# Optimization experiments

Measured on AMD Instinct MI355X. Metric: run time of the kernel, lower is better.

Reference implementation:

```python
import jax, jax.numpy as jnp
import numpy as np

SHIFT, REDUCE = 1, 2
B, L, E, H = 128, 64, 512, 512
T = 2 * L - 1  # valid binary-parse transition sequence length


def _make_transitions(rng):
    # Random *valid* shift-reduce sequences: L shifts, L-1 reduces, stack ends at 1.
    trans = np.zeros((B, T), dtype=np.int32)
    for b in range(B):
        stack, buf = 0, L
        for t in range(T):
            ops_left = T - t
            can_shift = buf > 0 and stack < ops_left
            can_reduce = stack >= 2
            if can_shift and can_reduce:
                act = SHIFT if rng.random() < 0.5 else REDUCE
            elif can_shift:
                act = SHIFT
            else:
                act = REDUCE
            if act == SHIFT:
                buf -= 1; stack += 1
            else:
                stack -= 1
            trans[b, t] = act
    return trans


def setup_inputs() -> dict:
    key = jax.random.key(0)
    k1, k2, k3, k4 = jax.random.split(key, 4)
    sentence = jax.random.normal(k1, (B, L, E), dtype=jnp.float32)
    transitions = jnp.asarray(_make_transitions(np.random.default_rng(0)))
    W_word = jax.random.normal(k2, (E, 2 * H), dtype=jnp.float32) / np.sqrt(E).astype(np.float32)
    b_word = jnp.zeros((2 * H,), dtype=jnp.float32)
    W_left = jax.random.normal(k3, (H, 5 * H), dtype=jnp.float32) / np.sqrt(H).astype(np.float32)
    W_right = jax.random.normal(k4, (H, 5 * H), dtype=jnp.float32) / np.sqrt(H).astype(np.float32)
    b_reduce = jnp.zeros((5 * H,), dtype=jnp.float32)
    return {"sentence": sentence, "transitions": transitions, "W_word": W_word,
            "b_word": b_word, "W_left": W_left, "W_right": W_right, "b_reduce": b_reduce}


def reference(sentence, transitions, W_word, b_word, W_left, W_right, b_reduce):
    Bx, Lx, _ = sentence.shape
    Hx = W_left.shape[0]
    Tx = transitions.shape[1]
    # word projection (no_batch_norm=True, dropout=0 in this config)
    out = sentence @ W_word + b_word                      # [B, L, 2H]
    h_buf, c_buf = jnp.split(out, 2, axis=2)              # buffers, popped front-to-back
    rows = jnp.arange(Bx)
    ops_left_seq = jnp.arange(Tx, 0, -1, dtype=jnp.int32)
    init = (jnp.zeros((Bx, Lx, Hx), out.dtype),           # stack h
            jnp.zeros((Bx, Lx, Hx), out.dtype),           # stack c
            jnp.zeros((Bx,), jnp.int32),                  # stack ptr
            jnp.zeros((Bx,), jnp.int32))                  # buffer ptr

    def step(carry, xs):
        sh, sc, sp, bp = carry
        act, ops = xs
        act = jnp.where(sp > ops, REDUCE, act)            # forced reduce (discrete stack)
        is_red = act == REDUCE
        is_shf = act == SHIFT
        r_idx = jnp.clip(sp - 1, 0, Lx - 1)
        l_idx = jnp.clip(sp - 2, 0, Lx - 1)
        hl, cl = sh[rows, l_idx], sc[rows, l_idx]
        hr, cr = sh[rows, r_idx], sc[rows, r_idx]
        # TreeLSTM Reduce cell
        gates = hl @ W_left + hr @ W_right + b_reduce     # [B, 5H]
        g, i, f1, f2, o = jnp.split(gates, 5, axis=1)
        c_red = jnp.tanh(g) * jax.nn.sigmoid(i) + jax.nn.sigmoid(f1) * cl + jax.nn.sigmoid(f2) * cr
        h_red = jax.nn.sigmoid(o) * jnp.tanh(c_red)
        b_idx = jnp.clip(bp, 0, Lx - 1)
        h_shf, c_shf = h_buf[rows, b_idx], c_buf[rows, b_idx]
        w_idx = jnp.where(is_red, l_idx, jnp.clip(sp, 0, Lx - 1))
        h_cur, c_cur = sh[rows, w_idx], sc[rows, w_idx]
        m_red, m_shf = is_red[:, None], is_shf[:, None]
        wh = jnp.where(m_red, h_red, jnp.where(m_shf, h_shf, h_cur))
        wc = jnp.where(m_red, c_red, jnp.where(m_shf, c_shf, c_cur))
        sh = sh.at[rows, w_idx].set(wh)
        sc = sc.at[rows, w_idx].set(wc)
        sp = sp + is_shf.astype(jnp.int32) - is_red.astype(jnp.int32)
        bp = bp + is_shf.astype(jnp.int32)
        return (sh, sc, sp, bp), None

    (sh, sc, sp, bp), _ = jax.lax.scan(step, init, (transitions.T, ops_left_seq))
    return sh[rows, jnp.clip(sp - 1, 0, Lx - 1)]          # [B, H] top of each stack
```

## Files before the change

### kernel.cpp

```cpp
#include <hip/hip_runtime.h>
#include <hip/hip_bf16.h>


#define Bn 128
#define Ln 64
#define En 512
#define Hn 512
#define Tn 127
#define LEAF_ROWS (Bn*Ln)
#define NODE_ROWS (Bn*(Ln-1))
#define TOT_ROWS (LEAF_ROWS+NODE_ROWS)
#define NLVL 64
#define NXCD 8
#define CAPX 512
#define NBLK 512
#define FPAD 16
#define MAXRANK 96
#define SPIN_CAP (1<<22)
#define WLDS_BYTES 65536
#define PART_BYTES (4*2*16*20*4)
#define DYN_BYTES (WLDS_BYTES + PART_BYTES)

#define OFF_CENSUS 0
#define OFF_RANK   (OFF_CENSUS + NXCD*FPAD)
#define OFF_SFLAG  (OFF_RANK + NBLK*FPAD)
#define OFF_SGEN   (OFF_SFLAG + NBLK*FPAD)
#define OFF_FX     (OFF_SGEN + FPAD)
#define OFF_GX     (OFF_FX + NXCD*MAXRANK*FPAD)
#define BAR_INTS   (OFF_GX + NXCD*FPAD)

typedef __attribute__((ext_vector_type(8))) short bf16x8;
typedef __attribute__((ext_vector_type(4))) float f32x4;

static __device__ __forceinline__ float bf2f(unsigned short u){
  unsigned v = ((unsigned)u) << 16;
  float f; __builtin_memcpy(&f, &v, 4); return f;
}
static __device__ __forceinline__ unsigned short f2bf(float f){
  unsigned u; __builtin_memcpy(&u, &f, 4);
  u = u + 0x7FFFu + ((u >> 16) & 1u);
  return (unsigned short)(u >> 16);
}
static __device__ __forceinline__ float sigm(float x){
  return 1.0f / (1.0f + __expf(-x));
}
static __device__ __forceinline__ float tanh_fast(float x){
  x = fminf(fmaxf(x, -15.0f), 15.0f);
  float t = __expf(2.0f * x);
  return (t - 1.0f) / (t + 1.0f);
}
static __device__ __forceinline__ int xcc_id(){
  unsigned v;
  asm volatile("s_getreg_b32 %0, hwreg(HW_REG_XCC_ID)" : "=s"(v));
  return (int)(v & 7);
}

static __device__ __forceinline__ void xcd_barrier(int* bar, int x, int rank, int nx, int epoch){
  __syncthreads();
  int* fx = bar + OFF_FX + x * MAXRANK * FPAD;
  int* gx = bar + OFF_GX + x * FPAD;
  int nxl = min(nx, MAXRANK);
  if (rank == 0){
    for (int i = threadIdx.x + 1; i < nxl; i += 256){
      int c = 0;
      while (__hip_atomic_load(&fx[i * FPAD], __ATOMIC_RELAXED, __HIP_MEMORY_SCOPE_AGENT) < epoch && c < SPIN_CAP){
        __builtin_amdgcn_s_sleep(1); ++c;
      }
    }
    __syncthreads();
    if (threadIdx.x == 0)
      __hip_atomic_store(gx, epoch, __ATOMIC_RELAXED, __HIP_MEMORY_SCOPE_AGENT);
  } else {
    if (threadIdx.x == 0){
      __hip_atomic_store(&fx[rank * FPAD], epoch, __ATOMIC_RELAXED, __HIP_MEMORY_SCOPE_AGENT);
      int c = 0;
      while (__hip_atomic_load(gx, __ATOMIC_RELAXED, __HIP_MEMORY_SCOPE_AGENT) < epoch && c < SPIN_CAP){
        __builtin_amdgcn_s_sleep(2); ++c;
      }
    }
    __syncthreads();
  }
  asm volatile("" ::: "memory");
}


__global__ void cvt_vec4(const float4* __restrict__ x, ushort4* __restrict__ y, int n4){
  int i = blockIdx.x * 256 + threadIdx.x;
  if (i < n4){
    float4 v = x[i];
    ushort4 o;
    o.x = f2bf(v.x); o.y = f2bf(v.y); o.z = f2bf(v.z); o.w = f2bf(v.w);
    y[i] = o;
  }
}

__global__ void transpose_cvt(const float* __restrict__ src, unsigned short* __restrict__ dstT,
                              int CS, int DS, int koff){
  __shared__ float tile[32][33];
  int c0 = blockIdx.x * 32, r0 = blockIdx.y * 32;
  int tx = threadIdx.x, ty = threadIdx.y;
  for (int i = ty; i < 32; i += 8) tile[i][tx] = src[(size_t)(r0 + i) * CS + c0 + tx];
  __syncthreads();
  for (int i = ty; i < 32; i += 8)
    dstT[(size_t)(c0 + i) * DS + koff + r0 + tx] = f2bf(tile[tx][i]);
}

__global__ void precompute_ctrl(const int* __restrict__ trans,
                                int* __restrict__ srcL, int* __restrict__ srcR,
                                int* __restrict__ dstv, int* __restrict__ cnt,
                                int* __restrict__ outsrc, int* __restrict__ bar){
  __shared__ int stk[Bn][Ln + 1];
  __shared__ int scnt[NXCD * NLVL];
  __shared__ int smaxl[NXCD];
  int b = threadIdx.x;
  for (int i = b; i < NXCD * NLVL; i += 128) scnt[i] = 0;
  if (b < NXCD) smaxl[b] = 0;
  for (int i = b; i < BAR_INTS; i += 128) bar[i] = 0;
  __syncthreads();
  int x = b & 7;
  int sp = 0, bp = 0, nodecnt = 0;
  int act_next = trans[b * Tn];
  for (int t = 0; t < Tn; t++){
    int act = act_next;
    if (t + 1 < Tn) act_next = trans[b * Tn + t + 1];
    int ops = Tn - t;
    if (sp > ops) act = 2;
    if (act == 2){
      int R = stk[b][sp - 1], L = stk[b][sp - 2];
      int lvl = max(R >> 20, L >> 20) + 1;
      int slot = atomicAdd(&scnt[x * NLVL + lvl], 1);
      int base = (x * NLVL + lvl) * CAPX + slot;
      srcL[base] = (L & 0xFFFFF) * Hn;
      srcR[base] = (R & 0xFFFFF) * Hn;
      int noderow = LEAF_ROWS + b * (Ln - 1) + nodecnt;
      dstv[base] = noderow * Hn;
      stk[b][sp - 2] = noderow | (lvl << 20);
      sp -= 1; nodecnt++;
    } else {
      stk[b][sp] = b * Ln + min(bp, Ln - 1);
      sp += 1; bp += 1;
    }
  }
  int root = stk[b][max(sp - 1, 0)];
  outsrc[b] = (root & 0xFFFFF) * Hn;
  atomicMax(&smaxl[x], root >> 20);
  __syncthreads();
  for (int i = b; i < NXCD * NLVL; i += 128) cnt[i] = scnt[i];
  if (b < NXCD) cnt[NXCD * NLVL + b] = smaxl[b];
}

__global__ __launch_bounds__(256) void word_gemm(
    const unsigned short* __restrict__ SB, const unsigned short* __restrict__ WwT,
    const float* __restrict__ b_word,
    unsigned short* __restrict__ HB, float* __restrict__ CF){
  int nt = blockIdx.x;
  int mt = blockIdx.y;
  int tid = threadIdx.x, w = tid >> 6, lane = tid & 63;
  int wm = w >> 1, wn = w & 1;
  int rc = lane & 15, lg = lane >> 4;
  const unsigned short* ap0 = SB + (size_t)(mt * 64 + wm * 32 + rc) * En + lg * 8;
  const unsigned short* ap1 = ap0 + (size_t)16 * En;
  const unsigned short* bp0 = WwT + (size_t)(nt * 128 + wn * 64 + rc) * En + lg * 8;
  f32x4 acc[2][4];
  #pragma unroll
  for (int h = 0; h < 2; h++)
    #pragma unroll
    for (int nb = 0; nb < 4; nb++) acc[h][nb] = (f32x4){0.f,0.f,0.f,0.f};
  #pragma unroll 4
  for (int k0 = 0; k0 < En; k0 += 32){
    bf16x8 a0 = *(const bf16x8*)(ap0 + k0);
    bf16x8 a1 = *(const bf16x8*)(ap1 + k0);
    #pragma unroll
    for (int nb = 0; nb < 4; nb++){
      bf16x8 bb = *(const bf16x8*)(bp0 + (size_t)nb * 16 * En + k0);
      acc[0][nb] = __builtin_amdgcn_mfma_f32_16x16x32_bf16(a0, bb, acc[0][nb], 0, 0, 0);
      acc[1][nb] = __builtin_amdgcn_mfma_f32_16x16x32_bf16(a1, bb, acc[1][nb], 0, 0, 0);
    }
  }
  #pragma unroll
  for (int nb = 0; nb < 4; nb++){
    int col = nt * 128 + wn * 64 + nb * 16 + rc;
    float bw = b_word[col];
    #pragma unroll
    for (int h = 0; h < 2; h++){
      #pragma unroll
      for (int q = 0; q < 4; q++){
        int row = mt * 64 + wm * 32 + h * 16 + lg * 4 + q;
        float v = acc[h][nb][q] + bw;
        if (col < Hn) HB[(size_t)row * Hn + col] = f2bf(v);
        else          CF[(size_t)row * Hn + (col - Hn)] = v;
      }
    }
  }
}

template<bool LDSB>
static __device__ __forceinline__ void tile64(
    int u0, int t, int nr, const int* __restrict__ sL, const int* __restrict__ sR,
    const int* __restrict__ dl,
    unsigned short* __restrict__ HB, float* __restrict__ CF,
    const unsigned short* __restrict__ WT, const float* __restrict__ b_red,
    const unsigned short* __restrict__ wlds, int rc, int lg)
{
  int base = t * 64;
  int offL[4], offR[4];
  #pragma unroll
  for (int m = 0; m < 4; m++){
    int i = min(base + m * 16 + rc, nr - 1);
    offL[m] = sL[i]; offR[m] = sR[i];
  }
  f32x4 acc[5][4];
  #pragma unroll
  for (int g = 0; g < 5; g++)
    #pragma unroll
    for (int m = 0; m < 4; m++) acc[g][m] = (f32x4){0.f,0.f,0.f,0.f};

  int bswz = (rc & 7) << 3;
  const unsigned short* gb = WT + (size_t)(u0 + rc) * 1024 + lg * 8;

  bf16x8 a_cur[4], b_cur[3];
  #pragma unroll
  for (int m = 0; m < 4; m++) a_cur[m] = *(const bf16x8*)(HB + offL[m] + lg * 8);
  #pragma unroll
  for (int g = 0; g < 3; g++)
    b_cur[g] = *(const bf16x8*)(gb + (size_t)(g + 2) * (512 * 1024));

  #pragma unroll 4
  for (int j = 0; j < 32; ++j){
    bf16x8 a_nxt[4], b_nxt[3];
    if (j < 31){
      int kn = (j + 1) * 32 + lg * 8;
      #pragma unroll
      for (int m = 0; m < 4; m++){
        const unsigned short* ap = (j + 1 < 16) ? (HB + offL[m] + kn) : (HB + offR[m] + (kn - 512));
        a_nxt[m] = *(const bf16x8*)ap;
      }
      #pragma unroll
      for (int g = 0; g < 3; g++)
        b_nxt[g] = *(const bf16x8*)(gb + (size_t)(g + 2) * (512 * 1024) + (j + 1) * 32);
    }
    int k = j * 32 + lg * 8;
    #pragma unroll
    for (int g = 0; g < 2; g++){
      bf16x8 bb;
      if (LDSB) bb = *(const bf16x8*)&wlds[(size_t)(g * 16 + rc) * 1024 + (k ^ bswz)];
      else      bb = *(const bf16x8*)(gb + (size_t)g * (512 * 1024) + j * 32);
      #pragma unroll
      for (int m = 0; m < 4; m++)
        acc[g][m] = __builtin_amdgcn_mfma_f32_16x16x32_bf16(a_cur[m], bb, acc[g][m], 0, 0, 0);
    }
    #pragma unroll
    for (int g = 0; g < 3; g++){
      #pragma unroll
      for (int m = 0; m < 4; m++)
        acc[g + 2][m] = __builtin_amdgcn_mfma_f32_16x16x32_bf16(a_cur[m], b_cur[g], acc[g + 2][m], 0, 0, 0);
    }
    #pragma unroll
    for (int m = 0; m < 4; m++) a_cur[m] = a_nxt[m];
    #pragma unroll
    for (int g = 0; g < 3; g++) b_cur[g] = b_nxt[g];
  }
  int colu = u0 + rc;
  float bs[5];
  #pragma unroll
  for (int g = 0; g < 5; g++) bs[g] = b_red[g * Hn + colu];
  #pragma unroll
  for (int m = 0; m < 4; m++){
    #pragma unroll
    for (int q = 0; q < 4; q++){
      int i = base + m * 16 + lg * 4 + q;
      if (i < nr){
        int oL = sL[i], oR = sR[i], oD = dl[i];
        float gv = tanh_fast(acc[0][m][q] + bs[0]);
        float iv = sigm(acc[1][m][q] + bs[1]);
        float f1 = sigm(acc[2][m][q] + bs[2]);
        float f2 = sigm(acc[3][m][q] + bs[3]);
        float ov = sigm(acc[4][m][q] + bs[4]);
        float cl = __builtin_nontemporal_load(CF + oL + colu);
        float cr = __builtin_nontemporal_load(CF + oR + colu);
        float cv = gv * iv + f1 * cl + f2 * cr;
        float hv = ov * tanh_fast(cv);
        __builtin_nontemporal_store(cv, CF + oD + colu);
        HB[oD + colu] = f2bf(hv);
      }
    }
  }
}

static __device__ __forceinline__ void tile16(
    int u0, int t, int nr, const int* __restrict__ sL, const int* __restrict__ sR,
    const int* __restrict__ dl,
    unsigned short* __restrict__ HB, float* __restrict__ CF,
    const unsigned short* __restrict__ WT, const float* __restrict__ b_red,
    const unsigned short* __restrict__ wlds, float (*part)[2][16][20],
    int tid, int w, int rc, int lg)
{
  int base = t * 16;
  int i0 = min(base + rc, nr - 1);
  int offA = (w >= 2) ? sR[i0] : sL[i0];
  int k0 = w * 256;
  int abase = (w >= 2) ? (k0 - 512) : k0;
  const unsigned short* ap = HB + offA + abase + lg * 8;
  int bswz = (rc & 7) << 3;
  const unsigned short* gb = WT + (size_t)(u0 + rc) * 1024;

  f32x4 acc[5];
  #pragma unroll
  for (int g = 0; g < 5; g++) acc[g] = (f32x4){0.f,0.f,0.f,0.f};

  bf16x8 a_cur = *(const bf16x8*)ap;
  bf16x8 b_cur[3];
  #pragma unroll
  for (int g = 0; g < 3; g++)
    b_cur[g] = *(const bf16x8*)(gb + (size_t)(g + 2) * (512 * 1024) + k0 + lg * 8);

  #pragma unroll
  for (int j = 0; j < 8; ++j){
    bf16x8 a_nxt, b_nxt[3];
    if (j < 7){
      a_nxt = *(const bf16x8*)(ap + (j + 1) * 32);
      #pragma unroll
      for (int g = 0; g < 3; g++)
        b_nxt[g] = *(const bf16x8*)(gb + (size_t)(g + 2) * (512 * 1024) + k0 + (j + 1) * 32 + lg * 8);
    }
    int k = k0 + j * 32 + lg * 8;
    #pragma unroll
    for (int g = 0; g < 2; g++){
      bf16x8 bb = *(const bf16x8*)&wlds[(size_t)(g * 16 + rc) * 1024 + (k ^ bswz)];
      acc[g] = __builtin_amdgcn_mfma_f32_16x16x32_bf16(a_cur, bb, acc[g], 0, 0, 0);
    }
    #pragma unroll
    for (int g = 0; g < 3; g++)
      acc[g + 2] = __builtin_amdgcn_mfma_f32_16x16x32_bf16(a_cur, b_cur[g], acc[g + 2], 0, 0, 0);
    a_cur = a_nxt;
    #pragma unroll
    for (int g = 0; g < 3; g++) b_cur[g] = b_nxt[g];
  }
  int er = tid >> 4, eu = tid & 15;
  float sg[5];
  #pragma unroll
  for (int r = 0; r < 3; ++r){
    int ng = (r < 2) ? 2 : 1;
    #pragma unroll
    for (int gi = 0; gi < 2; ++gi){
      if (gi < ng){
        int g = r * 2 + gi;
        #pragma unroll
        for (int q = 0; q < 4; q++) part[w][gi][lg * 4 + q][rc] = acc[g][q];
      }
    }
    __syncthreads();
    #pragma unroll
    for (int gi = 0; gi < 2; ++gi){
      if (gi < ng)
        sg[r * 2 + gi] = part[0][gi][er][eu] + part[1][gi][er][eu]
                       + part[2][gi][er][eu] + part[3][gi][er][eu];
    }
    __syncthreads();
  }
  int i = base + er;
  if (i < nr){
    int colu = u0 + eu;
    int oL = sL[i], oR = sR[i], oD = dl[i];
    float gv = tanh_fast(sg[0] + b_red[colu]);
    float iv = sigm(sg[1] + b_red[Hn + colu]);
    float f1 = sigm(sg[2] + b_red[2 * Hn + colu]);
    float f2 = sigm(sg[3] + b_red[3 * Hn + colu]);
    float ov = sigm(sg[4] + b_red[4 * Hn + colu]);
    float cl = __builtin_nontemporal_load(CF + oL + colu);
    float cr = __builtin_nontemporal_load(CF + oR + colu);
    float cv = gv * iv + f1 * cl + f2 * cr;
    float hv = ov * tanh_fast(cv);
    __builtin_nontemporal_store(cv, CF + oD + colu);
    HB[oD + colu] = f2bf(hv);
  }
  __syncthreads();
}

extern __shared__ char dynbuf[];

__global__ __launch_bounds__(256, 2) void tree_kernel(
    unsigned short* __restrict__ HB, float* __restrict__ CF,
    const unsigned short* __restrict__ WT, const float* __restrict__ b_red,
    const int* __restrict__ srcL, const int* __restrict__ srcR,
    const int* __restrict__ dstv, const int* __restrict__ cnt,
    const int* __restrict__ outsrc, float* __restrict__ out, int* bar){
  unsigned short* wlds = (unsigned short*)dynbuf;
  float (*part)[2][16][20] = (float(*)[2][16][20])(dynbuf + WLDS_BYTES);
  int bid = blockIdx.x;
  int tid = threadIdx.x, w = tid >> 6, lane = tid & 63;
  int rc = lane & 15, lg = lane >> 4;

  int x = xcc_id();
  if (tid == 0){
    int r = __hip_atomic_fetch_add(&bar[OFF_CENSUS + x * FPAD], 1,
                                   __ATOMIC_RELAXED, __HIP_MEMORY_SCOPE_AGENT);
    __hip_atomic_store(&bar[OFF_RANK + bid * FPAD], r, __ATOMIC_RELAXED, __HIP_MEMORY_SCOPE_AGENT);
  }
  __syncthreads();
  int rank = min(__hip_atomic_load(&bar[OFF_RANK + bid * FPAD], __ATOMIC_RELAXED, __HIP_MEMORY_SCOPE_AGENT),
                 MAXRANK - 1);
  int ub = rank & 31;
  int u0 = ub * 16;

  for (int gg = tid; gg < 4096; gg += 256){
    int row = gg >> 7;
    int k = (gg & 127) * 8;
    int u = row & 15, g = row >> 4;
    bf16x8 v = *(const bf16x8*)(WT + (size_t)(g * 512 + u0 + u) * 1024 + k);
    int kx = k ^ ((u & 7) << 3);
    *(bf16x8*)&wlds[(size_t)row * 1024 + kx] = v;
  }
  __syncthreads();

  {
    int* sfl  = bar + OFF_SFLAG;
    int* sgen = bar + OFF_SGEN;
    if (bid == 0){
      for (int i = tid; i < NBLK; i += 256){
        if (i){
          int c = 0;
          while (__hip_atomic_load(&sfl[i * FPAD], __ATOMIC_RELAXED, __HIP_MEMORY_SCOPE_AGENT) == 0 && c < SPIN_CAP){
            __builtin_amdgcn_s_sleep(1); ++c;
          }
        }
      }
      __syncthreads();
      if (tid == 0) __hip_atomic_store(sgen, 1, __ATOMIC_RELAXED, __HIP_MEMORY_SCOPE_AGENT);
    } else {
      if (tid == 0){
        __hip_atomic_store(&sfl[bid * FPAD], 1, __ATOMIC_RELAXED, __HIP_MEMORY_SCOPE_AGENT);
        int c = 0;
        while (__hip_atomic_load(sgen, __ATOMIC_RELAXED, __HIP_MEMORY_SCOPE_AGENT) == 0 && c < SPIN_CAP){
          __builtin_amdgcn_s_sleep(2); ++c;
        }
      }
      __syncthreads();
    }
  }
  int nx = max(__hip_atomic_load(&bar[OFF_CENSUS + x * FPAD], __ATOMIC_RELAXED, __HIP_MEMORY_SCOPE_AGENT), 1);

  int maxlvl = cnt[NXCD * NLVL + x];
  int epoch = 1;
  for (int lvl = 1; lvl <= maxlvl; ++lvl, ++epoch){
    int nr = cnt[x * NLVL + lvl];
    const int* sL = srcL + (x * NLVL + lvl) * CAPX;
    const int* sR = srcR + (x * NLVL + lvl) * CAPX;
    const int* dl = dstv + (x * NLVL + lvl) * CAPX;
    if (nr > 0){
      if (nx >= 32){
        int nstr = (nx - 1 - ub) / 32 + 1;
        int stripe = rank >> 5;
        if (nr >= 128){
          int ntl = (nr + 63) >> 6;
          for (int t = stripe * 4 + w; t < ntl; t += nstr * 4)
            tile64<true>(u0, t, nr, sL, sR, dl, HB, CF, WT, b_red, wlds, rc, lg);
        } else {
          int ntl16 = (nr + 15) >> 4;
          for (int t = stripe; t < ntl16; t += nstr)
            tile16(u0, t, nr, sL, sR, dl, HB, CF, WT, b_red, wlds, part, tid, w, rc, lg);
        }
      } else {
        int ntl = (nr + 63) >> 6;
        int nwv = nx * 4, wid = rank * 4 + w;
        int ntask = ntl * 32;
        for (int task = wid; task < ntask; task += nwv)
          tile64<false>((task / ntl) * 16, task % ntl, nr, sL, sR, dl, HB, CF, WT, b_red, wlds, rc, lg);
      }
    }
    xcd_barrier(bar, x, rank, nx, epoch);
  }

  for (int j = rank; j < 16; j += min(nx, MAXRANK)){
    int b = x + 8 * j;
    int src = outsrc[b];
    out[b * Hn + tid]       = bf2f(HB[src + tid]);
    out[b * Hn + tid + 256] = bf2f(HB[src + tid + 256]);
  }
}

extern "C" void kernel_launch(void* const* d_in, const int* in_sizes, int n_in,
                              void* d_out, int out_size, void* d_ws, size_t ws_size,
                              hipStream_t stream){
  (void)in_sizes; (void)n_in; (void)out_size; (void)ws_size;
  const float* sentence = (const float*)d_in[0];
  const int*   trans    = (const int*)d_in[1];
  const float* W_word   = (const float*)d_in[2];
  const float* b_word   = (const float*)d_in[3];
  const float* W_left   = (const float*)d_in[4];
  const float* W_right  = (const float*)d_in[5];
  const float* b_red    = (const float*)d_in[6];

  char* ws = (char*)d_ws;
  size_t off = 0;
  auto alloc = [&](size_t bytes) -> void* {
    void* p = ws + off;
    off += (bytes + 255) & ~((size_t)255);
    return p;
  };
  unsigned short* HB  = (unsigned short*)alloc((size_t)TOT_ROWS * Hn * 2);
  float*          CF  = (float*)alloc((size_t)TOT_ROWS * Hn * 4);
  unsigned short* WT  = (unsigned short*)alloc((size_t)2560 * 1024 * 2);
  unsigned short* SB  = (unsigned short*)alloc((size_t)LEAF_ROWS * En * 2);
  unsigned short* WwT = (unsigned short*)alloc((size_t)1024 * En * 2);
  int* srcL   = (int*)alloc((size_t)NXCD * NLVL * CAPX * 4);
  int* srcR   = (int*)alloc((size_t)NXCD * NLVL * CAPX * 4);
  int* dstv   = (int*)alloc((size_t)NXCD * NLVL * CAPX * 4);
  int* cnt    = (int*)alloc((size_t)(NXCD * NLVL + NXCD) * 4);
  int* outsrc = (int*)alloc((size_t)Bn * 4);
  int* bar    = (int*)alloc((size_t)BAR_INTS * 4);
  float* outp = (float*)d_out;

  hipFuncSetAttribute(reinterpret_cast<const void*>(tree_kernel),
                      hipFuncAttributeMaxDynamicSharedMemorySize, DYN_BYTES);

  cvt_vec4<<<(LEAF_ROWS * En / 4) / 256, 256, 0, stream>>>((const float4*)sentence, (ushort4*)SB, LEAF_ROWS * En / 4);
  transpose_cvt<<<dim3(1024 / 32, En / 32), dim3(32, 8), 0, stream>>>(W_word, WwT, 1024, En, 0);
  transpose_cvt<<<dim3(2560 / 32, Hn / 32), dim3(32, 8), 0, stream>>>(W_left, WT, 2560, 1024, 0);
  transpose_cvt<<<dim3(2560 / 32, Hn / 32), dim3(32, 8), 0, stream>>>(W_right, WT, 2560, 1024, 512);
  precompute_ctrl<<<1, 128, 0, stream>>>(trans, srcL, srcR, dstv, cnt, outsrc, bar);
  word_gemm<<<dim3(8, LEAF_ROWS / 64), 256, 0, stream>>>(SB, WwT, b_word, HB, CF);
  tree_kernel<<<NBLK, 256, DYN_BYTES, stream>>>(HB, CF, WT, b_red, srcL, srcR, dstv, cnt, outsrc, outp, bar);
}
```

Baseline: 598.3 us.

## Deepen load pipelines, prefetch next-level indices, hoist cell-state loads, tighten barrier spin

The word GEMM and the tile16 inner loop now use a three-stage register ring that prefetches two k-steps ahead instead of one. Both tree tiles load the child cell states (cl/cr) before the MFMA loop, so that latency overlaps compute. tile16 also cuts its LDS reduction from three sync rounds to two by enlarging the partial buffer. Before each XCD barrier, the next level's index gathers for tile16 are issued early. The barrier spin drops or shortens its sleeps to cut wake-up latency, which adds register pressure and memory polling traffic.

Result: slower. 776.4 us (+29.8%).

```diff
diff --git a/kernel.cpp b/kernel.cpp
--- a/kernel.cpp
+++ b/kernel.cpp
@@ -17,8 +17,9 @@
 #define FPAD 16
 #define MAXRANK 96
 #define SPIN_CAP (1<<22)
+#define GATE_STRIDE (512*1024)
 #define WLDS_BYTES 65536
-#define PART_BYTES (4*2*16*20*4)
+#define PART_BYTES (4*3*16*20*4)
 #define DYN_BYTES (WLDS_BYTES + PART_BYTES)
 
 #define OFF_CENSUS 0
@@ -64,7 +65,7 @@
     for (int i = threadIdx.x + 1; i < nxl; i += 256){
       int c = 0;
       while (__hip_atomic_load(&fx[i * FPAD], __ATOMIC_RELAXED, __HIP_MEMORY_SCOPE_AGENT) < epoch && c < SPIN_CAP){
-        __builtin_amdgcn_s_sleep(1); ++c;
+        ++c;
       }
     }
     __syncthreads();
@@ -75,7 +76,7 @@
       __hip_atomic_store(&fx[rank * FPAD], epoch, __ATOMIC_RELAXED, __HIP_MEMORY_SCOPE_AGENT);
       int c = 0;
       while (__hip_atomic_load(gx, __ATOMIC_RELAXED, __HIP_MEMORY_SCOPE_AGENT) < epoch && c < SPIN_CAP){
-        __builtin_amdgcn_s_sleep(2); ++c;
+        __builtin_amdgcn_s_sleep(1); ++c;
       }
     }
     __syncthreads();
@@ -166,15 +167,31 @@
   for (int h = 0; h < 2; h++)
     #pragma unroll
     for (int nb = 0; nb < 4; nb++) acc[h][nb] = (f32x4){0.f,0.f,0.f,0.f};
-  #pragma unroll 4
-  for (int k0 = 0; k0 < En; k0 += 32){
-    bf16x8 a0 = *(const bf16x8*)(ap0 + k0);
-    bf16x8 a1 = *(const bf16x8*)(ap1 + k0);
+
+  bf16x8 aS0[3], aS1[3], bS[4][3];
+  #pragma unroll
+  for (int s = 0; s < 2; s++){
+    aS0[s] = *(const bf16x8*)(ap0 + s * 32);
+    aS1[s] = *(const bf16x8*)(ap1 + s * 32);
+    #pragma unroll
+    for (int nb = 0; nb < 4; nb++)
+      bS[nb][s] = *(const bf16x8*)(bp0 + (size_t)nb * 16 * En + s * 32);
+  }
+  #pragma unroll
+  for (int j = 0; j < 16; ++j){
+    const int cur = j % 3, n2 = (j + 2) % 3;
+    if (j < 14){
+      int kn = (j + 2) * 32;
+      aS0[n2] = *(const bf16x8*)(ap0 + kn);
+      aS1[n2] = *(const bf16x8*)(ap1 + kn);
+      #pragma unroll
+      for (int nb = 0; nb < 4; nb++)
+        bS[nb][n2] = *(const bf16x8*)(bp0 + (size_t)nb * 16 * En + kn);
+    }
     #pragma unroll
     for (int nb = 0; nb < 4; nb++){
-      bf16x8 bb = *(const bf16x8*)(bp0 + (size_t)nb * 16 * En + k0);
-      acc[0][nb] = __builtin_amdgcn_mfma_f32_16x16x32_bf16(a0, bb, acc[0][nb], 0, 0, 0);
-      acc[1][nb] = __builtin_amdgcn_mfma_f32_16x16x32_bf16(a1, bb, acc[1][nb], 0, 0, 0);
+      acc[0][nb] = __builtin_amdgcn_mfma_f32_16x16x32_bf16(aS0[cur], bS[nb][cur], acc[0][nb], 0, 0, 0);
+      acc[1][nb] = __builtin_amdgcn_mfma_f32_16x16x32_bf16(aS1[cur], bS[nb][cur], acc[1][nb], 0, 0, 0);
     }
   }
   #pragma unroll
@@ -209,6 +226,17 @@
     int i = min(base + m * 16 + rc, nr - 1);
     offL[m] = sL[i]; offR[m] = sR[i];
   }
+  int colu = u0 + rc;
+  float clv[4][4], crv[4][4];
+  #pragma unroll
+  for (int m = 0; m < 4; m++){
+    #pragma unroll
+    for (int q = 0; q < 4; q++){
+      int ic = min(base + m * 16 + lg * 4 + q, nr - 1);
+      clv[m][q] = __builtin_nontemporal_load(CF + sL[ic] + colu);
+      crv[m][q] = __builtin_nontemporal_load(CF + sR[ic] + colu);
+    }
+  }
   f32x4 acc[5][4];
   #pragma unroll
   for (int g = 0; g < 5; g++)
@@ -223,7 +251,7 @@
   for (int m = 0; m < 4; m++) a_cur[m] = *(const bf16x8*)(HB + offL[m] + lg * 8);
   #pragma unroll
   for (int g = 0; g < 3; g++)
-    b_cur[g] = *(const bf16x8*)(gb + (size_t)(g + 2) * (512 * 1024));
+    b_cur[g] = *(const bf16x8*)(gb + (size_t)(g + 2) * GATE_STRIDE);
 
   #pragma unroll 4
   for (int j = 0; j < 32; ++j){
@@ -237,14 +265,14 @@
       }
       #pragma unroll
       for (int g = 0; g < 3; g++)
-        b_nxt[g] = *(const bf16x8*)(gb + (size_t)(g + 2) * (512 * 1024) + (j + 1) * 32);
+        b_nxt[g] = *(const bf16x8*)(gb + (size_t)(g + 2) * GATE_STRIDE + (j + 1) * 32);
     }
     int k = j * 32 + lg * 8;
     #pragma unroll
     for (int g = 0; g < 2; g++){
       bf16x8 bb;
       if (LDSB) bb = *(const bf16x8*)&wlds[(size_t)(g * 16 + rc) * 1024 + (k ^ bswz)];
-      else      bb = *(const bf16x8*)(gb + (size_t)g * (512 * 1024) + j * 32);
+      else      bb = *(const bf16x8*)(gb + (size_t)g * GATE_STRIDE + j * 32);
       #pragma unroll
       for (int m = 0; m < 4; m++)
         acc[g][m] = __builtin_amdgcn_mfma_f32_16x16x32_bf16(a_cur[m], bb, acc[g][m], 0, 0, 0);
@@ -260,7 +288,6 @@
     #pragma unroll
     for (int g = 0; g < 3; g++) b_cur[g] = b_nxt[g];
   }
-  int colu = u0 + rc;
   float bs[5];
   #pragma unroll
   for (int g = 0; g < 5; g++) bs[g] = b_red[g * Hn + colu];
@@ -270,15 +297,13 @@
     for (int q = 0; q < 4; q++){
       int i = base + m * 16 + lg * 4 + q;
       if (i < nr){
-        int oL = sL[i], oR = sR[i], oD = dl[i];
+        int oD = dl[i];
         float gv = tanh_fast(acc[0][m][q] + bs[0]);
         float iv = sigm(acc[1][m][q] + bs[1]);
         float f1 = sigm(acc[2][m][q] + bs[2]);
         float f2 = sigm(acc[3][m][q] + bs[3]);
         float ov = sigm(acc[4][m][q] + bs[4]);
-        float cl = __builtin_nontemporal_load(CF + oL + colu);
-        float cr = __builtin_nontemporal_load(CF + oR + colu);
-        float cv = gv * iv + f1 * cl + f2 * cr;
+        float cv = gv * iv + f1 * clv[m][q] + f2 * crv[m][q];
         float hv = ov * tanh_fast(cv);
         __builtin_nontemporal_store(cv, CF + oD + colu);
         HB[oD + colu] = f2bf(hv);
@@ -292,12 +317,25 @@
     const int* __restrict__ dl,
     unsigned short* __restrict__ HB, float* __restrict__ CF,
     const unsigned short* __restrict__ WT, const float* __restrict__ b_red,
-    const unsigned short* __restrict__ wlds, float (*part)[2][16][20],
-    int tid, int w, int rc, int lg)
+    const unsigned short* __restrict__ wlds, float (*part)[3][16][20],
+    int tid, int w, int rc, int lg,
+    bool up, int pre_offA, int pre_oL, int pre_oR, int pre_oD)
 {
   int base = t * 16;
-  int i0 = min(base + rc, nr - 1);
-  int offA = (w >= 2) ? sR[i0] : sL[i0];
+  int er = tid >> 4, eu = tid & 15;
+  int offA, oL, oR, oD;
+  if (up){
+    offA = pre_offA; oL = pre_oL; oR = pre_oR; oD = pre_oD;
+  } else {
+    int i0 = min(base + rc, nr - 1);
+    offA = (w >= 2) ? sR[i0] : sL[i0];
+    int ie = min(base + er, nr - 1);
+    oL = sL[ie]; oR = sR[ie]; oD = dl[ie];
+  }
+  int colu = u0 + eu;
+  float cl = __builtin_nontemporal_load(CF + oL + colu);
+  float cr = __builtin_nontemporal_load(CF + oR + colu);
+
   int k0 = w * 256;
   int abase = (w >= 2) ? (k0 - 512) : k0;
   const unsigned short* ap = HB + offA + abase + lg * 8;
@@ -308,67 +346,59 @@
   #pragma unroll
   for (int g = 0; g < 5; g++) acc[g] = (f32x4){0.f,0.f,0.f,0.f};
 
-  bf16x8 a_cur = *(const bf16x8*)ap;
-  bf16x8 b_cur[3];
-  #pragma unroll
-  for (int g = 0; g < 3; g++)
-    b_cur[g] = *(const bf16x8*)(gb + (size_t)(g + 2) * (512 * 1024) + k0 + lg * 8);
-
+  bf16x8 aS[3], bS[3][3];
+  #pragma unroll
+  for (int s = 0; s < 2; s++){
+    aS[s] = *(const bf16x8*)(ap + s * 32);
+    #pragma unroll
+    for (int g = 0; g < 3; g++)
+      bS[g][s] = *(const bf16x8*)(gb + (size_t)(g + 2) * GATE_STRIDE + k0 + s * 32 + lg * 8);
+  }
   #pragma unroll
   for (int j = 0; j < 8; ++j){
-    bf16x8 a_nxt, b_nxt[3];
-    if (j < 7){
-      a_nxt = *(const bf16x8*)(ap + (j + 1) * 32);
+    const int cur = j % 3, n2 = (j + 2) % 3;
+    if (j < 6){
+      aS[n2] = *(const bf16x8*)(ap + (j + 2) * 32);
       #pragma unroll
       for (int g = 0; g < 3; g++)
-        b_nxt[g] = *(const bf16x8*)(gb + (size_t)(g + 2) * (512 * 1024) + k0 + (j + 1) * 32 + lg * 8);
+        bS[g][n2] = *(const bf16x8*)(gb + (size_t)(g + 2) * GATE_STRIDE + k0 + (j + 2) * 32 + lg * 8);
     }
     int k = k0 + j * 32 + lg * 8;
     #pragma unroll
     for (int g = 0; g < 2; g++){
       bf16x8 bb = *(const bf16x8*)&wlds[(size_t)(g * 16 + rc) * 1024 + (k ^ bswz)];
-      acc[g] = __builtin_amdgcn_mfma_f32_16x16x32_bf16(a_cur, bb, acc[g], 0, 0, 0);
+      acc[g] = __builtin_amdgcn_mfma_f32_16x16x32_bf16(aS[cur], bb, acc[g], 0, 0, 0);
     }
     #pragma unroll
     for (int g = 0; g < 3; g++)
-      acc[g + 2] = __builtin_amdgcn_mfma_f32_16x16x32_bf16(a_cur, b_cur[g], acc[g + 2], 0, 0, 0);
-    a_cur = a_nxt;
-    #pragma unroll
-    for (int g = 0; g < 3; g++) b_cur[g] = b_nxt[g];
-  }
-  int er = tid >> 4, eu = tid & 15;
+      acc[g + 2] = __builtin_amdgcn_mfma_f32_16x16x32_bf16(aS[cur], bS[g][cur], acc[g + 2], 0, 0, 0);
+  }
   float sg[5];
   #pragma unroll
-  for (int r = 0; r < 3; ++r){
-    int ng = (r < 2) ? 2 : 1;
-    #pragma unroll
-    for (int gi = 0; gi < 2; ++gi){
-      if (gi < ng){
-        int g = r * 2 + gi;
-        #pragma unroll
-        for (int q = 0; q < 4; q++) part[w][gi][lg * 4 + q][rc] = acc[g][q];
-      }
-    }
-    __syncthreads();
-    #pragma unroll
-    for (int gi = 0; gi < 2; ++gi){
-      if (gi < ng)
-        sg[r * 2 + gi] = part[0][gi][er][eu] + part[1][gi][er][eu]
-                       + part[2][gi][er][eu] + part[3][gi][er][eu];
-    }
-    __syncthreads();
-  }
+  for (int g = 0; g < 3; g++)
+    #pragma unroll
+    for (int q = 0; q < 4; q++) part[w][g][lg * 4 + q][rc] = acc[g][q];
+  __syncthreads();
+  #pragma unroll
+  for (int g = 0; g < 3; g++)
+    sg[g] = part[0][g][er][eu] + part[1][g][er][eu] + part[2][g][er][eu] + part[3][g][er][eu];
+  __syncthreads();
+  #pragma unroll
+  for (int g = 0; g < 2; g++)
+    #pragma unroll
+    for (int q = 0; q < 4; q++) part[w][g][lg * 4 + q][rc] = acc[3 + g][q];
+  __syncthreads();
+  #pragma unroll
+  for (int g = 0; g < 2; g++)
+    sg[3 + g] = part[0][g][er][eu] + part[1][g][er][eu] + part[2][g][er][eu] + part[3][g][er][eu];
+
   int i = base + er;
   if (i < nr){
-    int colu = u0 + eu;
-    int oL = sL[i], oR = sR[i], oD = dl[i];
     float gv = tanh_fast(sg[0] + b_red[colu]);
     float iv = sigm(sg[1] + b_red[Hn + colu]);
     float f1 = sigm(sg[2] + b_red[2 * Hn + colu]);
     float f2 = sigm(sg[3] + b_red[3 * Hn + colu]);
     float ov = sigm(sg[4] + b_red[4 * Hn + colu]);
-    float cl = __builtin_nontemporal_load(CF + oL + colu);
-    float cr = __builtin_nontemporal_load(CF + oR + colu);
     float cv = gv * iv + f1 * cl + f2 * cr;
     float hv = ov * tanh_fast(cv);
     __builtin_nontemporal_store(cv, CF + oD + colu);
@@ -386,10 +416,11 @@
     const int* __restrict__ dstv, const int* __restrict__ cnt,
     const int* __restrict__ outsrc, float* __restrict__ out, int* bar){
   unsigned short* wlds = (unsigned short*)dynbuf;
-  float (*part)[2][16][20] = (float(*)[2][16][20])(dynbuf + WLDS_BYTES);
+  float (*part)[3][16][20] = (float(*)[3][16][20])(dynbuf + WLDS_BYTES);
   int bid = blockIdx.x;
   int tid = threadIdx.x, w = tid >> 6, lane = tid & 63;
   int rc = lane & 15, lg = lane >> 4;
+  int er = tid >> 4;
 
   int x = xcc_id();
   if (tid == 0){
@@ -442,15 +473,17 @@
 
   int maxlvl = cnt[NXCD * NLVL + x];
   int epoch = 1;
+  int pre_offA = 0, pre_oL = 0, pre_oR = 0, pre_oD = 0;
+  bool have_pre = false;
   for (int lvl = 1; lvl <= maxlvl; ++lvl, ++epoch){
     int nr = cnt[x * NLVL + lvl];
     const int* sL = srcL + (x * NLVL + lvl) * CAPX;
     const int* sR = srcR + (x * NLVL + lvl) * CAPX;
     const int* dl = dstv + (x * NLVL + lvl) * CAPX;
+    int stripe = rank >> 5;
     if (nr > 0){
       if (nx >= 32){
         int nstr = (nx - 1 - ub) / 32 + 1;
-        int stripe = rank >> 5;
         if (nr >= 128){
           int ntl = (nr + 63) >> 6;
           for (int t = stripe * 4 + w; t < ntl; t += nstr * 4)
@@ -458,7 +491,8 @@
         } else {
           int ntl16 = (nr + 15) >> 4;
           for (int t = stripe; t < ntl16; t += nstr)
-            tile16(u0, t, nr, sL, sR, dl, HB, CF, WT, b_red, wlds, part, tid, w, rc, lg);
+            tile16(u0, t, nr, sL, sR, dl, HB, CF, WT, b_red, wlds, part, tid, w, rc, lg,
+                   have_pre && (t == stripe), pre_offA, pre_oL, pre_oR, pre_oD);
         }
       } else {
         int ntl = (nr + 63) >> 6;
@@ -466,6 +500,23 @@
         int ntask = ntl * 32;
         for (int task = wid; task < ntask; task += nwv)
           tile64<false>((task / ntl) * 16, task % ntl, nr, sL, sR, dl, HB, CF, WT, b_red, wlds, rc, lg);
+      }
+    }
+    have_pre = false;
+    if (lvl < maxlvl && nx >= 32){
+      int nr2 = cnt[x * NLVL + lvl + 1];
+      if (nr2 > 0 && nr2 < 128){
+        const int* sL2 = srcL + (x * NLVL + lvl + 1) * CAPX;
+        const int* sR2 = srcR + (x * NLVL + lvl + 1) * CAPX;
+        const int* dl2 = dstv + (x * NLVL + lvl + 1) * CAPX;
+        int ntl2 = (nr2 + 15) >> 4;
+        if (stripe < ntl2){
+          int i0 = min(stripe * 16 + rc, nr2 - 1);
+          pre_offA = (w >= 2) ? sR2[i0] : sL2[i0];
+          int ie = min(stripe * 16 + er, nr2 - 1);
+          pre_oL = sL2[ie]; pre_oR = sR2[ie]; pre_oD = dl2[ie];
+          have_pre = true;
+        }
       }
     }
     xcd_barrier(bar, x, rank, nx, epoch);
```
